# Kernel tuning notes

Hardware: AMD Instinct MI355X
Metric: run time of the kernel (lower is better)

## Reference

```python
import jax, jax.numpy as jnp
import numpy as np

NUM_HEADS = 16


def _bayes_w(mu, rho, eps):
    # reparameterized weight sample: w = mu + softplus(rho) * eps
    return mu + jax.nn.softplus(rho) * eps


def setup_inputs() -> dict:
    key = jax.random.key(0)
    ks = jax.random.split(key, 12)
    B, N, C = 4, 2048, 1024
    x = jax.random.normal(ks[0], (B, N, C), jnp.float32)
    w_scale = 0.02
    q_w = jax.random.normal(ks[1], (C, C), jnp.float32) * w_scale
    k_w = jax.random.normal(ks[2], (C, C), jnp.float32) * w_scale
    v_mu = jax.random.normal(ks[3], (C, C), jnp.float32) * w_scale
    v_rho = jax.random.normal(ks[4], (C, C), jnp.float32) * 0.1 - 3.0
    v_eps = jax.random.normal(ks[5], (C, C), jnp.float32)
    proj_mu = jax.random.normal(ks[6], (C, C), jnp.float32) * w_scale
    proj_rho = jax.random.normal(ks[7], (C, C), jnp.float32) * 0.1 - 3.0
    proj_eps = jax.random.normal(ks[8], (C, C), jnp.float32)
    pb_mu = jax.random.normal(ks[9], (C,), jnp.float32) * w_scale
    pb_rho = jax.random.normal(ks[10], (C,), jnp.float32) * 0.1 - 3.0
    pb_eps = jax.random.normal(ks[11], (C,), jnp.float32)
    return {"x": x, "q_w": q_w, "k_w": k_w, "v_mu": v_mu, "v_rho": v_rho,
            "v_eps": v_eps, "proj_mu": proj_mu, "proj_rho": proj_rho,
            "proj_eps": proj_eps, "pb_mu": pb_mu, "pb_rho": pb_rho,
            "pb_eps": pb_eps}


def reference(x, q_w, k_w, v_mu, v_rho, v_eps, proj_mu, proj_rho, proj_eps,
              pb_mu, pb_rho, pb_eps):
    B, N, C = x.shape
    H = NUM_HEADS
    D = C // H
    scale = D ** -0.5
    v_w = _bayes_w(v_mu, v_rho, v_eps)
    # projections (torch Linear: y = x @ W.T)
    q = (x @ q_w.T).reshape(B, N, H, D).transpose(0, 2, 1, 3)  # [B,H,N,D]
    k = (x @ k_w.T).reshape(B, N, H, D).transpose(0, 2, 1, 3)
    v = (x @ v_w.T).reshape(B, N, H, D).transpose(0, 2, 1, 3)
    attn = jax.nn.softmax(jnp.einsum("bhnd,bhmd->bhnm", q * scale, k), axis=-1)
    out = jnp.einsum("bhnm,bhmd->bhnd", attn, v)
    out = out.transpose(0, 2, 1, 3).reshape(B, N, C)
    p_w = _bayes_w(proj_mu, proj_rho, proj_eps)
    p_b = _bayes_w(pb_mu, pb_rho, pb_eps)
    return out @ p_w.T + p_b
```

## Files before the change

### kernel.cpp

```cpp
#include <hip/hip_runtime.h>
#include <hip/hip_bf16.h>
#include <cstdint>
#include <math.h>

typedef __bf16 bf16;
typedef __bf16 bf16x8 __attribute__((ext_vector_type(8)));
typedef __bf16 bf16x4 __attribute__((ext_vector_type(4)));
typedef float  f32x4 __attribute__((ext_vector_type(4)));

#define LOG2E 1.4426950408889634f

#if __has_builtin(__builtin_amdgcn_exp2f)
#define EXP2(x) __builtin_amdgcn_exp2f(x)
#else
#define EXP2(x) exp2f(x)
#endif

#define AS1 __attribute__((address_space(1)))
#define AS3 __attribute__((address_space(3)))

__device__ __forceinline__ void gload_lds16(const bf16* g, bf16* l) {
    __builtin_amdgcn_global_load_lds((AS1 void*)g, (AS3 void*)l, 16, 0, 0);
}

__device__ __forceinline__ float softplus_f(float r) {
    return (r > 15.f) ? r : log1pf(expf(r));
}

#define MFMA16(a, b, c) __builtin_amdgcn_mfma_f32_16x16x32_bf16((a), (b), (c), 0, 0, 0)
#define CFENCE asm volatile("" ::: "memory")

__global__ __launch_bounds__(256)
void prep_kernel(const float* __restrict__ x, bf16* __restrict__ xb,
                 const float* __restrict__ q_w, const float* __restrict__ k_w,
                 bf16* __restrict__ wqkv,
                 const float* __restrict__ v_mu, const float* __restrict__ v_rho,
                 const float* __restrict__ v_eps,
                 const float* __restrict__ p_mu, const float* __restrict__ p_rho,
                 const float* __restrict__ p_eps, bf16* __restrict__ pwb,
                 const float* __restrict__ pb_mu, const float* __restrict__ pb_rho,
                 const float* __restrict__ pb_eps, float* __restrict__ p_b) {
    const int Wsz = 1024 * 1024;
    int blk = blockIdx.x;
    if (blk < 8192) {
        int i = blk * 256 + threadIdx.x;
        float4 v = ((const float4*)x)[i];
        bf16 o[4] = {(bf16)v.x, (bf16)v.y, (bf16)v.z, (bf16)v.w};
        *(uint64_t*)&xb[i * 4] = *(uint64_t*)o;
    } else if (blk < 10240) {
        const float* src = (blk < 9216) ? q_w : k_w;
        bf16* dst = (blk < 9216) ? wqkv : wqkv + Wsz;
        int i = ((blk - 8192) & 1023) * 256 + threadIdx.x;
        float4 v = ((const float4*)src)[i];
        bf16 o[4] = {(bf16)v.x, (bf16)v.y, (bf16)v.z, (bf16)v.w};
        *(uint64_t*)&dst[i * 4] = *(uint64_t*)o;
    } else if (blk < 12288) {
        const bool isv = blk < 11264;
        const float* mu  = isv ? v_mu  : p_mu;
        const float* rho = isv ? v_rho : p_rho;
        const float* eps = isv ? v_eps : p_eps;
        bf16* dst = isv ? wqkv + 2 * Wsz : pwb;
        int i = ((blk - 10240) & 1023) * 256 + threadIdx.x;
        float4 m = ((const float4*)mu)[i];
        float4 r = ((const float4*)rho)[i];
        float4 e = ((const float4*)eps)[i];
        bf16 o[4] = {(bf16)(m.x + softplus_f(r.x) * e.x),
                     (bf16)(m.y + softplus_f(r.y) * e.y),
                     (bf16)(m.z + softplus_f(r.z) * e.z),
                     (bf16)(m.w + softplus_f(r.w) * e.w)};
        *(uint64_t*)&dst[i * 4] = *(uint64_t*)o;
    } else {
        int i = threadIdx.x;
        float4 m = ((const float4*)pb_mu)[i];
        float4 r = ((const float4*)pb_rho)[i];
        float4 e = ((const float4*)pb_eps)[i];
        float4 o;
        o.x = m.x + softplus_f(r.x) * e.x;
        o.y = m.y + softplus_f(r.y) * e.y;
        o.z = m.z + softplus_f(r.z) * e.z;
        o.w = m.w + softplus_f(r.w) * e.w;
        ((float4*)p_b)[i] = o;
    }
}

template <typename OutT>
__global__ __launch_bounds__(512, 2)
void gemm_8ph(const bf16* __restrict__ A, const bf16* __restrict__ W,
              OutT* __restrict__ C, const float* __restrict__ bias,
              int M, int N, int K, float q_scale, int q_cols) {
    __shared__ bf16 sA[2][256 * 64];
    __shared__ bf16 sB[2][256 * 64];

    const int lane  = threadIdx.x & 63;
    const int wv    = threadIdx.x >> 6;
    const int wr    = wv >> 2;
    const int wc    = wv & 3;
    const int col16 = lane & 15, quad = lane >> 4;

    const int nwg = gridDim.x * gridDim.y;
    int bidl = blockIdx.y * gridDim.x + blockIdx.x;
    if ((nwg & 7) == 0) bidl = (bidl & 7) * (nwg >> 3) + (bidl >> 3);
    const int m0 = (bidl / gridDim.x) * 256;
    const int n0 = (bidl % gridDim.x) * 256;

    const int st_r = lane >> 2;
    const int st_c = ((lane & 3) * 8) ^ (((lane >> 5) & 1) << 4);
    const bf16* Asrc = A + (size_t)(m0 + st_r) * K + st_c;
    const bf16* Bsrc = W + (size_t)(n0 + st_r) * K + st_c;
    const size_t rgK = (size_t)16 * K;

    const int lp = col16 * 32 + ((quad * 8) ^ (((col16 >> 3) & 1) << 4));

    f32x4 acc[2][2][4][2] = {};
    const int NT = K >> 6;

#define STAGE_A(buf, half, kt) do { \
        const bf16* s_ = Asrc + (size_t)((half) * 8 + wv) * rgK + ((size_t)(kt) << 6); \
        bf16* l_ = &sA[buf][((half) * 8 + wv) * 1024]; \
        gload_lds16(s_, l_); gload_lds16(s_ + 32, l_ + 512); } while (0)
#define STAGE_B(buf, half, kt) do { \
        const bf16* s_ = Bsrc + (size_t)((half) * 8 + wv) * rgK + ((size_t)(kt) << 6); \
        bf16* l_ = &sB[buf][((half) * 8 + wv) * 1024]; \
        gload_lds16(s_, l_); gload_lds16(s_ + 32, l_ + 512); } while (0)

    STAGE_A(0, 0, 0); STAGE_B(0, 0, 0); STAGE_B(0, 1, 0); STAGE_A(0, 1, 0);
    if (NT > 1) { STAGE_A(1, 0, 1); STAGE_B(1, 0, 1); STAGE_B(1, 1, 1); }
    if (NT > 1) asm volatile("s_waitcnt vmcnt(6)" ::: "memory");
    else        asm volatile("s_waitcnt vmcnt(0)" ::: "memory");
    __builtin_amdgcn_s_barrier();
    CFENCE;

    bf16x8 afr[4][2], bfr0[2][2], bfr1[2][2];

    for (int t = 0; t < NT; ++t) {
        const int d = t & 1;

#pragma unroll
        for (int mm = 0; mm < 4; ++mm)
#pragma unroll
            for (int ks = 0; ks < 2; ++ks)
                afr[mm][ks] = *(const bf16x8*)&sA[d][((2 * mm + wr) * 2 + ks) * 512 + lp];
#pragma unroll
        for (int nn = 0; nn < 2; ++nn)
#pragma unroll
            for (int ks = 0; ks < 2; ++ks)
                bfr0[nn][ks] = *(const bf16x8*)&sB[d][((nn * 4 + wc) * 2 + ks) * 512 + lp];
        if (t + 1 < NT) STAGE_A(d ^ 1, 1, t + 1);
        CFENCE; __builtin_amdgcn_s_barrier(); CFENCE;
        __builtin_amdgcn_s_setprio(1);
#pragma unroll
        for (int mm = 0; mm < 4; ++mm)
#pragma unroll
            for (int nn = 0; nn < 2; ++nn) {
                acc[0][0][mm][nn] = MFMA16(afr[mm][0], bfr0[nn][0], acc[0][0][mm][nn]);
                acc[0][0][mm][nn] = MFMA16(afr[mm][1], bfr0[nn][1], acc[0][0][mm][nn]);
            }
        __builtin_amdgcn_s_setprio(0);
        CFENCE; __builtin_amdgcn_s_barrier(); CFENCE;

#pragma unroll
        for (int nn = 0; nn < 2; ++nn)
#pragma unroll
            for (int ks = 0; ks < 2; ++ks)
                bfr1[nn][ks] = *(const bf16x8*)&sB[d][((8 + nn * 4 + wc) * 2 + ks) * 512 + lp];
        if (t + 2 < NT) STAGE_A(d, 0, t + 2);
        CFENCE; __builtin_amdgcn_s_barrier(); CFENCE;
        __builtin_amdgcn_s_setprio(1);
#pragma unroll
        for (int mm = 0; mm < 4; ++mm)
#pragma unroll
            for (int nn = 0; nn < 2; ++nn) {
                acc[0][1][mm][nn] = MFMA16(afr[mm][0], bfr1[nn][0], acc[0][1][mm][nn]);
                acc[0][1][mm][nn] = MFMA16(afr[mm][1], bfr1[nn][1], acc[0][1][mm][nn]);
            }
        __builtin_amdgcn_s_setprio(0);
        CFENCE; __builtin_amdgcn_s_barrier(); CFENCE;

#pragma unroll
        for (int mm = 0; mm < 4; ++mm)
#pragma unroll
            for (int ks = 0; ks < 2; ++ks)
                afr[mm][ks] = *(const bf16x8*)&sA[d][((8 + 2 * mm + wr) * 2 + ks) * 512 + lp];
        if (t + 2 < NT) STAGE_B(d, 0, t + 2);
        CFENCE; __builtin_amdgcn_s_barrier(); CFENCE;
        __builtin_amdgcn_s_setprio(1);
#pragma unroll
        for (int mm = 0; mm < 4; ++mm)
#pragma unroll
            for (int nn = 0; nn < 2; ++nn) {
                acc[1][1][mm][nn] = MFMA16(afr[mm][0], bfr1[nn][0], acc[1][1][mm][nn]);
                acc[1][1][mm][nn] = MFMA16(afr[mm][1], bfr1[nn][1], acc[1][1][mm][nn]);
            }
        __builtin_amdgcn_s_setprio(0);
        CFENCE; __builtin_amdgcn_s_barrier(); CFENCE;

        if (t + 2 < NT) STAGE_B(d, 1, t + 2);
        CFENCE; __builtin_amdgcn_s_barrier(); CFENCE;
        __builtin_amdgcn_s_setprio(1);
#pragma unroll
        for (int mm = 0; mm < 4; ++mm)
#pragma unroll
            for (int nn = 0; nn < 2; ++nn) {
                acc[1][0][mm][nn] = MFMA16(afr[mm][0], bfr0[nn][0], acc[1][0][mm][nn]);
                acc[1][0][mm][nn] = MFMA16(afr[mm][1], bfr0[nn][1], acc[1][0][mm][nn]);
            }
        __builtin_amdgcn_s_setprio(0);
        if (t + 2 < NT) asm volatile("s_waitcnt vmcnt(6)" ::: "memory");
        else            asm volatile("s_waitcnt vmcnt(0)" ::: "memory");
        __builtin_amdgcn_s_barrier();
        CFENCE;
    }
#undef STAGE_A
#undef STAGE_B

    const float scale = (n0 < q_cols) ? q_scale : 1.0f;
#pragma unroll
    for (int a = 0; a < 2; ++a)
#pragma unroll
        for (int b = 0; b < 2; ++b)
#pragma unroll
            for (int mm = 0; mm < 4; ++mm)
#pragma unroll
                for (int nn = 0; nn < 2; ++nn) {
                    int row = m0 + (a * 8 + 2 * mm + wr) * 16 + quad * 4;
                    int cc  = n0 + (b * 8 + nn * 4 + wc) * 16 + col16;
                    float bv = bias ? bias[cc] : 0.f;
#pragma unroll
                    for (int r = 0; r < 4; ++r)
                        C[(size_t)(row + r) * N + cc] = (OutT)(acc[a][b][mm][nn][r] * scale + bv);
                }
}

#define SWZ(row, ec) ((row) * 64 + ((ec) ^ (((row) & 7) << 3)))

__global__ __launch_bounds__(256, 2)
void attn_kernel(const bf16* __restrict__ QKV, bf16* __restrict__ O) {
    __shared__ bf16 sK[2][64 * 64];
    __shared__ bf16 sVt[64 * 64];
    __shared__ bf16 sP [256 * 64];

    const int lane = threadIdx.x & 63;
    const int wv   = threadIdx.x >> 6;
    const int col  = lane & 15, quad = lane >> 4;

    const int bid  = blockIdx.x;
    const int work = (bid & 7) * 64 + (bid >> 3);
    const int qt = work & 7, h = (work >> 3) & 15, b = work >> 7;

    const size_t rowQ0 = (size_t)b * 2048 + qt * 256;
    const bf16* Qg = QKV + rowQ0 * 3072 + h * 64;
    const bf16* Kg = QKV + (size_t)b * 2048 * 3072 + 1024 + h * 64;
    const bf16* Vg = QKV + (size_t)b * 2048 * 3072 + 2048 + h * 64;

    const int rloc = lane >> 3;
    const bf16* Kdma = Kg + (size_t)(wv * 16 + rloc) * 3072 + (((lane & 7) ^ rloc) * 8);

    gload_lds16(Kdma,                    &sK[0][(wv * 16) * 64]);
    gload_lds16(Kdma + (size_t)8 * 3072, &sK[0][(wv * 16 + 8) * 64]);

    const int dc0 = wv * 8, dc1 = 32 + wv * 8;
    bf16x8 vr0 = *(const bf16x8*)&Vg[(size_t)lane * 3072 + dc0];
    bf16x8 vr1 = *(const bf16x8*)&Vg[(size_t)lane * 3072 + dc1];

#pragma unroll
    for (int it = 0; it < 8; ++it) {
        int c = it * 256 + threadIdx.x;
        int row = c >> 3, ec = (c & 7) * 8;
        *(bf16x8*)&sP[SWZ(row, ec)] = *(const bf16x8*)&Qg[(size_t)row * 3072 + ec];
    }
    __syncthreads();
    bf16x8 qf[4][2];
#pragma unroll
    for (int mi = 0; mi < 4; ++mi)
#pragma unroll
        for (int ks = 0; ks < 2; ++ks)
            qf[mi][ks] = *(const bf16x8*)&sP[SWZ(wv * 64 + mi * 16 + col, ks * 32 + quad * 8)];

    f32x4 lsum[4] = {};
    f32x4 o[4][4] = {};
    const int cx = col & 7;

    for (int t = 0; t < 32; ++t) {
        const int p = t & 1;

#pragma unroll
        for (int j = 0; j < 8; ++j) sVt[SWZ(dc0 + j, lane)] = vr0[j];
#pragma unroll
        for (int j = 0; j < 8; ++j) sVt[SWZ(dc1 + j, lane)] = vr1[j];
        __syncthreads();

        if (t < 31) {
            const bf16* kn = Kdma + (size_t)(t * 64 + 64) * 3072;
            gload_lds16(kn,                    &sK[p ^ 1][(wv * 16) * 64]);
            gload_lds16(kn + (size_t)8 * 3072, &sK[p ^ 1][(wv * 16 + 8) * 64]);
        }

        bf16x8 kf0[4], kf1[4];
#pragma unroll
        for (int nj = 0; nj < 4; ++nj) {
            kf0[nj] = *(const bf16x8*)&sK[p][(nj * 16 + col) * 64 + ((quad ^ cx) * 8)];
            kf1[nj] = *(const bf16x8*)&sK[p][(nj * 16 + col) * 64 + (((quad ^ cx) ^ 4) * 8)];
        }

#pragma unroll
        for (int mi = 0; mi < 4; ++mi) {
            f32x4 st[4];
            __builtin_amdgcn_s_setprio(1);
#pragma unroll
            for (int nj = 0; nj < 4; ++nj) {
                f32x4 tacc = {0.f, 0.f, 0.f, 0.f};
                tacc = MFMA16(kf0[nj], qf[mi][0], tacc);
                tacc = MFMA16(kf1[nj], qf[mi][1], tacc);
                st[nj] = tacc;
            }
            __builtin_amdgcn_s_setprio(0);
#pragma unroll
            for (int nj = 0; nj < 4; ++nj) {
                f32x4 pv;
#pragma unroll
                for (int r = 0; r < 4; ++r) pv[r] = EXP2(st[nj][r]);
                lsum[mi] += pv;
                bf16x4 pk = {(bf16)pv[0], (bf16)pv[1], (bf16)pv[2], (bf16)pv[3]};
                *(bf16x4*)&sP[SWZ(wv * 64 + mi * 16 + col, nj * 16 + quad * 4)] = pk;
            }
        }

        if (t < 31) {
            const bf16* vn = Vg + (size_t)(t * 64 + 64 + lane) * 3072;
            vr0 = *(const bf16x8*)&vn[dc0];
            vr1 = *(const bf16x8*)&vn[dc1];
        }

        __builtin_amdgcn_s_setprio(1);
#pragma unroll
        for (int ks = 0; ks < 2; ++ks) {
            bf16x8 pf[4];
#pragma unroll
            for (int mi = 0; mi < 4; ++mi)
                pf[mi] = *(const bf16x8*)&sP[SWZ(wv * 64 + mi * 16 + col, ks * 32 + quad * 8)];
#pragma unroll
            for (int dj = 0; dj < 4; ++dj) {
                bf16x8 vf = *(const bf16x8*)&sVt[SWZ(dj * 16 + col, ks * 32 + quad * 8)];
#pragma unroll
                for (int mi = 0; mi < 4; ++mi)
                    o[mi][dj] = MFMA16(pf[mi], vf, o[mi][dj]);
            }
        }
        __builtin_amdgcn_s_setprio(0);
        __syncthreads();
    }

#pragma unroll
    for (int mi = 0; mi < 4; ++mi) {
        float l = lsum[mi][0] + lsum[mi][1] + lsum[mi][2] + lsum[mi][3];
        l += __shfl_xor(l, 16, 64);
        l += __shfl_xor(l, 32, 64);
#pragma unroll
        for (int r = 0; r < 4; ++r) {
            float inv = 1.f / __shfl(l, quad * 4 + r, 64);
            size_t row = rowQ0 + wv * 64 + mi * 16 + quad * 4 + r;
#pragma unroll
            for (int dj = 0; dj < 4; ++dj)
                O[row * 1024 + h * 64 + dj * 16 + col] = (bf16)(o[mi][dj][r] * inv);
        }
    }
}

extern "C" void kernel_launch(void* const* d_in, const int* in_sizes, int n_in,
                              void* d_out, int out_size, void* d_ws, size_t ws_size,
                              hipStream_t stream) {
    const float* x      = (const float*)d_in[0];
    const float* q_w    = (const float*)d_in[1];
    const float* k_w    = (const float*)d_in[2];
    const float* v_mu   = (const float*)d_in[3];
    const float* v_rho  = (const float*)d_in[4];
    const float* v_eps  = (const float*)d_in[5];
    const float* p_mu   = (const float*)d_in[6];
    const float* p_rho  = (const float*)d_in[7];
    const float* p_eps  = (const float*)d_in[8];
    const float* pb_mu  = (const float*)d_in[9];
    const float* pb_rho = (const float*)d_in[10];
    const float* pb_eps = (const float*)d_in[11];
    float* out = (float*)d_out;

    const size_t MB = (size_t)1 << 20;
    char* ws = (char*)d_ws;
    bf16*  xb   = (bf16*)(ws);
    bf16*  wqkv = (bf16*)(ws + 16 * MB);
    bf16*  pwb  = (bf16*)(ws + 22 * MB);
    float* p_b  = (float*)(ws + 24 * MB);
    bf16*  QKV  = (bf16*)(ws + 25 * MB);
    bf16*  Ab   = xb;

    prep_kernel<<<12289, 256, 0, stream>>>(x, xb, q_w, k_w, wqkv,
                                           v_mu, v_rho, v_eps,
                                           p_mu, p_rho, p_eps, pwb,
                                           pb_mu, pb_rho, pb_eps, p_b);

    gemm_8ph<bf16><<<dim3(12, 32), 512, 0, stream>>>(xb, wqkv, QKV, nullptr,
                                                     8192, 3072, 1024, 0.125f * LOG2E, 1024);

    attn_kernel<<<dim3(512), 256, 0, stream>>>(QKV, Ab);

    gemm_8ph<float><<<dim3(4, 32), 512, 0, stream>>>(Ab, pwb, out, p_b,
                                                     8192, 1024, 1024, 1.0f, 1024);
}
```

Baseline: 304.8 us.

## Use 256x128 tiles for output projection and stage GEMM epilogue through LDS

Templates the GEMM on BL so the output projection uses 256x128 tiles, which doubles its grid from 128 to 256 workgroups and fills more CUs. The epilogue now writes results into swizzled LDS and then stores full 16-byte rows back to global memory, instead of making scattered scalar stores. This trades extra LDS traffic and a barrier for coalesced writes. The smaller tile also gives each workgroup less reuse of the A operand.

```diff
diff --git a/kernel.cpp b/kernel.cpp
--- a/kernel.cpp
+++ b/kernel.cpp
@@ -83,13 +83,16 @@
     }
 }
 
-template <typename OutT>
+template <typename OutT, int BL>
 __global__ __launch_bounds__(512, 2)
 void gemm_8ph(const bf16* __restrict__ A, const bf16* __restrict__ W,
               OutT* __restrict__ C, const float* __restrict__ bias,
               int M, int N, int K, float q_scale, int q_cols) {
-    __shared__ bf16 sA[2][256 * 64];
-    __shared__ bf16 sB[2][256 * 64];
+    __shared__ __align__(16) char smem[131072];
+    bf16* sA = (bf16*)smem;
+    bf16* sB = (bf16*)(smem + 65536);
+    const int BN = 128 * BL;
+    const int SBB = BN * 64;
 
     const int lane  = threadIdx.x & 63;
     const int wv    = threadIdx.x >> 6;
@@ -101,7 +104,7 @@
     int bidl = blockIdx.y * gridDim.x + blockIdx.x;
     if ((nwg & 7) == 0) bidl = (bidl & 7) * (nwg >> 3) + (bidl >> 3);
     const int m0 = (bidl / gridDim.x) * 256;
-    const int n0 = (bidl % gridDim.x) * 256;
+    const int n0 = (bidl % gridDim.x) * BN;
 
     const int st_r = lane >> 2;
     const int st_c = ((lane & 3) * 8) ^ (((lane >> 5) & 1) << 4);
@@ -111,26 +114,35 @@
 
     const int lp = col16 * 32 + ((quad * 8) ^ (((col16 >> 3) & 1) << 4));
 
-    f32x4 acc[2][2][4][2] = {};
+    f32x4 acc[2][2][4][BL] = {};
     const int NT = K >> 6;
 
 #define STAGE_A(buf, half, kt) do { \
         const bf16* s_ = Asrc + (size_t)((half) * 8 + wv) * rgK + ((size_t)(kt) << 6); \
-        bf16* l_ = &sA[buf][((half) * 8 + wv) * 1024]; \
+        bf16* l_ = &sA[(buf) * 16384 + ((half) * 8 + wv) * 1024]; \
         gload_lds16(s_, l_); gload_lds16(s_ + 32, l_ + 512); } while (0)
 #define STAGE_B(buf, half, kt) do { \
-        const bf16* s_ = Bsrc + (size_t)((half) * 8 + wv) * rgK + ((size_t)(kt) << 6); \
-        bf16* l_ = &sB[buf][((half) * 8 + wv) * 1024]; \
-        gload_lds16(s_, l_); gload_lds16(s_ + 32, l_ + 512); } while (0)
+        if constexpr (BL == 2) { \
+            const bf16* s_ = Bsrc + (size_t)((half) * 8 + wv) * rgK + ((size_t)(kt) << 6); \
+            bf16* l_ = &sB[(buf) * SBB + ((half) * 8 + wv) * 1024]; \
+            gload_lds16(s_, l_); gload_lds16(s_ + 32, l_ + 512); \
+        } else { \
+            const int rg_ = wv >> 1, kc_ = wv & 1; \
+            const bf16* s_ = Bsrc + (size_t)((half) * 4 + rg_) * rgK + kc_ * 32 + ((size_t)(kt) << 6); \
+            gload_lds16(s_, &sB[(buf) * SBB + (((half) * 4 + rg_) * 2 + kc_) * 512]); \
+        } } while (0)
+#define WAIT_STEADY do { \
+        if constexpr (BL == 2) asm volatile("s_waitcnt vmcnt(6)" ::: "memory"); \
+        else                   asm volatile("s_waitcnt vmcnt(4)" ::: "memory"); } while (0)
 
     STAGE_A(0, 0, 0); STAGE_B(0, 0, 0); STAGE_B(0, 1, 0); STAGE_A(0, 1, 0);
     if (NT > 1) { STAGE_A(1, 0, 1); STAGE_B(1, 0, 1); STAGE_B(1, 1, 1); }
-    if (NT > 1) asm volatile("s_waitcnt vmcnt(6)" ::: "memory");
+    if (NT > 1) WAIT_STEADY;
     else        asm volatile("s_waitcnt vmcnt(0)" ::: "memory");
     __builtin_amdgcn_s_barrier();
     CFENCE;
 
-    bf16x8 afr[4][2], bfr0[2][2], bfr1[2][2];
+    bf16x8 afr[4][2], bfr0[BL][2], bfr1[BL][2];
 
     for (int t = 0; t < NT; ++t) {
         const int d = t & 1;
@@ -139,19 +151,19 @@
         for (int mm = 0; mm < 4; ++mm)
 #pragma unroll
             for (int ks = 0; ks < 2; ++ks)
-                afr[mm][ks] = *(const bf16x8*)&sA[d][((2 * mm + wr) * 2 + ks) * 512 + lp];
-#pragma unroll
-        for (int nn = 0; nn < 2; ++nn)
+                afr[mm][ks] = *(const bf16x8*)&sA[d * 16384 + ((2 * mm + wr) * 2 + ks) * 512 + lp];
+#pragma unroll
+        for (int nn = 0; nn < BL; ++nn)
 #pragma unroll
             for (int ks = 0; ks < 2; ++ks)
-                bfr0[nn][ks] = *(const bf16x8*)&sB[d][((nn * 4 + wc) * 2 + ks) * 512 + lp];
+                bfr0[nn][ks] = *(const bf16x8*)&sB[d * SBB + ((nn * 4 + wc) * 2 + ks) * 512 + lp];
         if (t + 1 < NT) STAGE_A(d ^ 1, 1, t + 1);
         CFENCE; __builtin_amdgcn_s_barrier(); CFENCE;
         __builtin_amdgcn_s_setprio(1);
 #pragma unroll
         for (int mm = 0; mm < 4; ++mm)
 #pragma unroll
-            for (int nn = 0; nn < 2; ++nn) {
+            for (int nn = 0; nn < BL; ++nn) {
                 acc[0][0][mm][nn] = MFMA16(afr[mm][0], bfr0[nn][0], acc[0][0][mm][nn]);
                 acc[0][0][mm][nn] = MFMA16(afr[mm][1], bfr0[nn][1], acc[0][0][mm][nn]);
             }
@@ -159,17 +171,17 @@
         CFENCE; __builtin_amdgcn_s_barrier(); CFENCE;
 
 #pragma unroll
-        for (int nn = 0; nn < 2; ++nn)
+        for (int nn = 0; nn < BL; ++nn)
 #pragma unroll
             for (int ks = 0; ks < 2; ++ks)
-                bfr1[nn][ks] = *(const bf16x8*)&sB[d][((8 + nn * 4 + wc) * 2 + ks) * 512 + lp];
+                bfr1[nn][ks] = *(const bf16x8*)&sB[d * SBB + ((4 * BL + nn * 4 + wc) * 2 + ks) * 512 + lp];
         if (t + 2 < NT) STAGE_A(d, 0, t + 2);
         CFENCE; __builtin_amdgcn_s_barrier(); CFENCE;
         __builtin_amdgcn_s_setprio(1);
 #pragma unroll
         for (int mm = 0; mm < 4; ++mm)
 #pragma unroll
-            for (int nn = 0; nn < 2; ++nn) {
+            for (int nn = 0; nn < BL; ++nn) {
                 acc[0][1][mm][nn] = MFMA16(afr[mm][0], bfr1[nn][0], acc[0][1][mm][nn]);
                 acc[0][1][mm][nn] = MFMA16(afr[mm][1], bfr1[nn][1], acc[0][1][mm][nn]);
             }
@@ -180,14 +192,14 @@
         for (int mm = 0; mm < 4; ++mm)
 #pragma unroll
             for (int ks = 0; ks < 2; ++ks)
-                afr[mm][ks] = *(const bf16x8*)&sA[d][((8 + 2 * mm + wr) * 2 + ks) * 512 + lp];
+                afr[mm][ks] = *(const bf16x8*)&sA[d * 16384 + ((8 + 2 * mm + wr) * 2 + ks) * 512 + lp];
         if (t + 2 < NT) STAGE_B(d, 0, t + 2);
         CFENCE; __builtin_amdgcn_s_barrier(); CFENCE;
         __builtin_amdgcn_s_setprio(1);
 #pragma unroll
         for (int mm = 0; mm < 4; ++mm)
 #pragma unroll
-            for (int nn = 0; nn < 2; ++nn) {
+            for (int nn = 0; nn < BL; ++nn) {
                 acc[1][1][mm][nn] = MFMA16(afr[mm][0], bfr1[nn][0], acc[1][1][mm][nn]);
                 acc[1][1][mm][nn] = MFMA16(afr[mm][1], bfr1[nn][1], acc[1][1][mm][nn]);
             }
@@ -200,18 +212,19 @@
 #pragma unroll
         for (int mm = 0; mm < 4; ++mm)
 #pragma unroll
-            for (int nn = 0; nn < 2; ++nn) {
+            for (int nn = 0; nn < BL; ++nn) {
                 acc[1][0][mm][nn] = MFMA16(afr[mm][0], bfr0[nn][0], acc[1][0][mm][nn]);
                 acc[1][0][mm][nn] = MFMA16(afr[mm][1], bfr0[nn][1], acc[1][0][mm][nn]);
             }
         __builtin_amdgcn_s_setprio(0);
-        if (t + 2 < NT) asm volatile("s_waitcnt vmcnt(6)" ::: "memory");
+        if (t + 2 < NT) WAIT_STEADY;
         else            asm volatile("s_waitcnt vmcnt(0)" ::: "memory");
         __builtin_amdgcn_s_barrier();
         CFENCE;
     }
 #undef STAGE_A
 #undef STAGE_B
+#undef WAIT_STEADY
 
     const float scale = (n0 < q_cols) ? q_scale : 1.0f;
 #pragma unroll
@@ -221,14 +234,28 @@
 #pragma unroll
             for (int mm = 0; mm < 4; ++mm)
 #pragma unroll
-                for (int nn = 0; nn < 2; ++nn) {
-                    int row = m0 + (a * 8 + 2 * mm + wr) * 16 + quad * 4;
-                    int cc  = n0 + (b * 8 + nn * 4 + wc) * 16 + col16;
-                    float bv = bias ? bias[cc] : 0.f;
-#pragma unroll
-                    for (int r = 0; r < 4; ++r)
-                        C[(size_t)(row + r) * N + cc] = (OutT)(acc[a][b][mm][nn][r] * scale + bv);
+                for (int nn = 0; nn < BL; ++nn) {
+                    const int cc = (b * 4 * BL + nn * 4 + wc) * 16 + col16;
+                    const float bv = bias ? bias[n0 + cc] : 0.f;
+                    const int cb = cc * (int)sizeof(OutT);
+#pragma unroll
+                    for (int r = 0; r < 4; ++r) {
+                        const int R = (a * 8 + 2 * mm + wr) * 16 + quad * 4 + r;
+                        *(OutT*)(smem + R * 512 + (cb ^ ((R & 7) << 4))) =
+                            (OutT)(acc[a][b][mm][nn][r] * scale + bv);
+                    }
                 }
+    __syncthreads();
+    char* Cb = (char*)C + ((size_t)m0 * N + n0) * sizeof(OutT);
+    const size_t rowB = (size_t)N * sizeof(OutT);
+    const int rr  = threadIdx.x >> 5;
+    const int cb0 = (threadIdx.x & 31) * 16;
+#pragma unroll
+    for (int j = 0; j < 16; ++j) {
+        const int R = j * 16 + rr;
+        uint4 v = *(const uint4*)(smem + R * 512 + (cb0 ^ ((R & 7) << 4)));
+        *(uint4*)(Cb + (size_t)R * rowB + cb0) = v;
+    }
 }
 
 #define SWZ(row, ec) ((row) * 64 + ((ec) ^ (((row) & 7) << 3)))
@@ -397,11 +424,11 @@
                                            p_mu, p_rho, p_eps, pwb,
                                            pb_mu, pb_rho, pb_eps, p_b);
 
-    gemm_8ph<bf16><<<dim3(12, 32), 512, 0, stream>>>(xb, wqkv, QKV, nullptr,
-                                                     8192, 3072, 1024, 0.125f * LOG2E, 1024);
+    gemm_8ph<bf16, 2><<<dim3(12, 32), 512, 0, stream>>>(xb, wqkv, QKV, nullptr,
+                                                        8192, 3072, 1024, 0.125f * LOG2E, 1024);
 
     attn_kernel<<<dim3(512), 256, 0, stream>>>(QKV, Ab);
 
-    gemm_8ph<float><<<dim3(4, 32), 512, 0, stream>>>(Ab, pwb, out, p_b,
-                                                     8192, 1024, 1024, 1.0f, 1024);
-}
+    gemm_8ph<float, 1><<<dim3(8, 32), 512, 0, stream>>>(Ab, pwb, out, p_b,
+                                                        8192, 1024, 1024, 1.0f, 1024);
+}
```

Result: faster. 291.3 us, median of 2 (-4.4%).
